# Kernel optimization log

Measured on AMD Instinct MI355X. Metric: run time of the kernel, lower is better.

The kernel has to match this reference:

```python
import jax, jax.numpy as jnp
import numpy as np

F_FRAMES = 128   # number of frames (seq_start_end rows)
P_PEDS = 32      # pedestrians per frame (uniform)
B = F_FRAMES * P_PEDS
E, H, BN, PM, M = 64, 128, 1024, 512, 1024
PRED_LEN = 12


def setup_inputs() -> dict:
    key = jax.random.key(0)
    ks = jax.random.split(key, 20)
    n = lambda k, s, sc=0.05: (jax.random.normal(k, s) * sc).astype(jnp.float32)
    starts = jnp.arange(F_FRAMES, dtype=jnp.int32) * P_PEDS
    seq_start_end = jnp.stack([starts, starts + P_PEDS], axis=1)
    return {
        "h0": n(ks[0], (1, B, H), 1.0),
        "c0": n(ks[1], (1, B, H), 1.0),
        "obs_final_pos": n(ks[2], (B, 2), 1.0),
        "obs_final_pos_rel": n(ks[3], (B, 2), 1.0),
        "W_emb": n(ks[4], (2, E)), "b_emb": jnp.zeros((E,), jnp.float32),
        "W_ih": n(ks[5], (4 * H, E)), "W_hh": n(ks[6], (4 * H, H)),
        "b_ih": jnp.zeros((4 * H,), jnp.float32), "b_hh": jnp.zeros((4 * H,), jnp.float32),
        "W_pos": n(ks[7], (H, 2)), "b_pos": jnp.zeros((2,), jnp.float32),
        "W_pe": n(ks[8], (2, E)), "b_pe": jnp.zeros((E,), jnp.float32),
        "W_p1": n(ks[9], (E + H, PM)), "b_p1": jnp.zeros((PM,), jnp.float32),
        "W_p2": n(ks[10], (PM, BN)), "b_p2": jnp.zeros((BN,), jnp.float32),
        "W_m1": n(ks[11], (H + BN, M)), "b_m1": jnp.zeros((M,), jnp.float32),
        "W_m2": n(ks[12], (M, H)), "b_m2": jnp.zeros((H,), jnp.float32),
        "seq_start_end": seq_start_end,
    }


def reference(h0, c0, obs_final_pos, obs_final_pos_rel,
              W_emb, b_emb, W_ih, W_hh, b_ih, b_hh, W_pos, b_pos,
              W_pe, b_pe, W_p1, b_p1, W_p2, b_p2, W_m1, b_m1, W_m2, b_m2,
              seq_start_end):
    Bn = h0.shape[1]
    F = seq_start_end.shape[0]
    P = Bn // F  # uniform frame size
    h, c = h0[0], c0[0]
    x0 = obs_final_pos_rel @ W_emb + b_emb  # decoder input embedding

    def step(carry, _):
        x, h, c, last_pos = carry
        # LSTM cell (PyTorch gate order i,f,g,o)
        gates = x @ W_ih.T + h @ W_hh.T + b_ih + b_hh  # (B, 4H)
        i, f, g, o = jnp.split(gates, 4, axis=-1)
        i, f, o = jax.nn.sigmoid(i), jax.nn.sigmoid(f), jax.nn.sigmoid(o)
        c_new = f * c + i * jnp.tanh(g)
        h_new = o * jnp.tanh(c_new)
        rel_pos = h_new @ W_pos + b_pos
        curr_pos = rel_pos + last_pos
        # PoolNet: per-frame pairwise rel-pos embed + MLP + max over neighbours j
        pos = curr_pos.reshape(F, P, 2)
        hf = h_new.reshape(F, P, H)
        rel = pos[:, None, :, :] - pos[:, :, None, :]  # rel[f,i,j] = pos_j - pos_i
        e = rel @ W_pe + b_pe  # (F,P,P,E)
        feat = jnp.concatenate(
            [e, jnp.broadcast_to(hf[:, None], (F, P, P, H))], axis=-1)  # h of j
        z = jax.nn.relu(feat @ W_p1 + b_p1)
        z = jax.nn.relu(z @ W_p2 + b_p2)  # (F,P,P,BN)
        pool_h = z.max(axis=2).reshape(Bn, BN)
        # hidden refresh MLP
        mi = jnp.concatenate([h_new, pool_h], axis=-1)
        nh = jax.nn.relu(mi @ W_m1 + b_m1)
        nh = jax.nn.relu(nh @ W_m2 + b_m2)
        x_new = rel_pos @ W_emb + b_emb
        return (x_new, nh, c_new, curr_pos), (curr_pos, rel_pos)

    _, (pred_seq, pred_seq_rel) = jax.lax.scan(
        jax.checkpoint(step), (x0, h, c, obs_final_pos), None, length=PRED_LEN)
    return pred_seq, pred_seq_rel
```

## Files before the change

kernel.cpp:

```cpp
#include <hip/hip_runtime.h>

#define NB 4096
#define HD 128
#define ED 64
#define NF 128
#define NP 32
#define TSTEPS 12

typedef __attribute__((ext_vector_type(8))) short short8;
typedef __attribute__((ext_vector_type(8))) __bf16 bf16x8;
typedef __attribute__((ext_vector_type(8))) _Float16 f16x8;
typedef __attribute__((ext_vector_type(4))) float f32x4;

#define MFMA16(a, b, c) __builtin_amdgcn_mfma_f32_16x16x32_bf16((a), (b), (c), 0, 0, 0)
#define MFMAH(a, b, c)  __builtin_amdgcn_mfma_f32_16x16x32_f16((a), (b), (c), 0, 0, 0)

__device__ __forceinline__ unsigned short f2bf(float f) {
  unsigned int x = __float_as_uint(f);
  x += 0x7fffu + ((x >> 16) & 1u);
  return (unsigned short)(x >> 16);
}

__device__ __forceinline__ float sigm(float x) { return 1.0f / (1.0f + expf(-x)); }


__global__ __launch_bounds__(256) void k_transpose_bf(const float* __restrict__ W,
                                                      unsigned short* __restrict__ Wt,
                                                      int K, int N) {
  __shared__ float t[32][33];
  int nb = blockIdx.x * 32, kb = blockIdx.y * 32;
  int tx = threadIdx.x & 31, ty = threadIdx.x >> 5;
  #pragma unroll
  for (int r = 0; r < 32; r += 8)
    t[ty + r][tx] = W[(size_t)(kb + ty + r) * N + nb + tx];
  __syncthreads();
  #pragma unroll
  for (int r = 0; r < 32; r += 8)
    Wt[(size_t)(nb + ty + r) * K + kb + tx] = f2bf(t[tx][ty + r]);
}

__global__ __launch_bounds__(256) void k_transpose_f16(const float* __restrict__ W,
                                                       _Float16* __restrict__ Wt,
                                                       int K, int N) {
  __shared__ float t[32][33];
  int nb = blockIdx.x * 32, kb = blockIdx.y * 32;
  int tx = threadIdx.x & 31, ty = threadIdx.x >> 5;
  #pragma unroll
  for (int r = 0; r < 32; r += 8)
    t[ty + r][tx] = W[(size_t)(kb + ty + r) * N + nb + tx];
  __syncthreads();
  #pragma unroll
  for (int r = 0; r < 32; r += 8)
    Wt[(size_t)(nb + ty + r) * K + kb + tx] = (_Float16)t[tx][ty + r];
}

__global__ __launch_bounds__(256) void k_pack_lstm_w(const float* __restrict__ Wih,
                                                     const float* __restrict__ Whh,
                                                     float* __restrict__ WihT,
                                                     float* __restrict__ WhhT) {
  int idx = blockIdx.x * 256 + threadIdx.x;
  if (idx < 64 * 512) { int k = idx >> 9, n = idx & 511; WihT[idx] = Wih[n * 64 + k]; }
  if (idx < 128 * 512) { int k = idx >> 9, n = idx & 511; WhhT[idx] = Whh[n * 128 + k]; }
}

__global__ __launch_bounds__(256) void k_pack_wpp(const float* __restrict__ Wpe,
                                                  const float* __restrict__ bpe,
                                                  const float* __restrict__ Wp1,
                                                  const float* __restrict__ bp1,
                                                  float* __restrict__ Wpp,
                                                  float* __restrict__ cvec) {
  int n = blockIdx.x * 256 + threadIdx.x;
  if (n >= 512) return;
  float s0 = 0.f, s1 = 0.f, sc = 0.f;
  for (int k = 0; k < 64; ++k) {
    float w = Wp1[k * 512 + n];
    s0 += Wpe[k] * w;
    s1 += Wpe[64 + k] * w;
    sc += bpe[k] * w;
  }
  Wpp[n * 2] = s0; Wpp[n * 2 + 1] = s1; cvec[n] = sc + bp1[n];
}

__global__ __launch_bounds__(256) void k_x0(const float* __restrict__ ofr,
                                            const float* __restrict__ Wemb,
                                            const float* __restrict__ bemb,
                                            float* __restrict__ x) {
  int idx = blockIdx.x * 256 + threadIdx.x;
  if (idx >= NB * ED) return;
  int row = idx >> 6, e = idx & 63;
  x[idx] = bemb[e] + ofr[row * 2] * Wemb[e] + ofr[row * 2 + 1] * Wemb[64 + e];
}


__global__ __launch_bounds__(256) void k1_lstm(
    const float* __restrict__ x, const float* __restrict__ hin, const float* __restrict__ cin,
    const float* __restrict__ WihT, const float* __restrict__ WhhT,
    const float* __restrict__ bih, const float* __restrict__ bhh,
    const float* __restrict__ Wpos, const float* __restrict__ bpos,
    const float* __restrict__ Wemb, const float* __restrict__ bemb,
    const float* __restrict__ lastpos,
    float* __restrict__ cout, float* __restrict__ hnew, unsigned short* __restrict__ mi,
    float* __restrict__ posout, float* __restrict__ xout,
    float* __restrict__ outc, float* __restrict__ outr) {
  __shared__ float xh[8][192];
  __shared__ float hnl[8][128];
  __shared__ float rp[8][2];
  int tid = threadIdx.x;
  int r0 = blockIdx.x * 8;
  for (int idx = tid; idx < 8 * 192; idx += 256) {
    int r = idx / 192, k = idx % 192;
    xh[r][k] = (k < 64) ? x[(r0 + r) * 64 + k] : hin[(r0 + r) * 128 + (k - 64)];
  }
  __syncthreads();
  int j = tid & 127, rg = tid >> 7;
  float acc0[4], acc1[4], acc2[4], acc3[4];
  {
    float b0 = bih[j] + bhh[j];
    float b1 = bih[128 + j] + bhh[128 + j];
    float b2 = bih[256 + j] + bhh[256 + j];
    float b3 = bih[384 + j] + bhh[384 + j];
    #pragma unroll
    for (int r = 0; r < 4; ++r) { acc0[r] = b0; acc1[r] = b1; acc2[r] = b2; acc3[r] = b3; }
  }
  for (int k = 0; k < 64; ++k) {
    float w0 = WihT[k * 512 + j], w1 = WihT[k * 512 + 128 + j],
          w2 = WihT[k * 512 + 256 + j], w3 = WihT[k * 512 + 384 + j];
    #pragma unroll
    for (int r = 0; r < 4; ++r) {
      float xv = xh[rg * 4 + r][k];
      acc0[r] += w0 * xv; acc1[r] += w1 * xv; acc2[r] += w2 * xv; acc3[r] += w3 * xv;
    }
  }
  for (int k = 0; k < 128; ++k) {
    float w0 = WhhT[k * 512 + j], w1 = WhhT[k * 512 + 128 + j],
          w2 = WhhT[k * 512 + 256 + j], w3 = WhhT[k * 512 + 384 + j];
    #pragma unroll
    for (int r = 0; r < 4; ++r) {
      float hv = xh[rg * 4 + r][64 + k];
      acc0[r] += w0 * hv; acc1[r] += w1 * hv; acc2[r] += w2 * hv; acc3[r] += w3 * hv;
    }
  }
  #pragma unroll
  for (int r = 0; r < 4; ++r) {
    int row = r0 + rg * 4 + r;
    float ig = sigm(acc0[r]), fg = sigm(acc1[r]), gg = tanhf(acc2[r]), og = sigm(acc3[r]);
    float cn = fg * cin[row * 128 + j] + ig * gg;
    float hv = og * tanhf(cn);
    cout[row * 128 + j] = cn;
    hnew[row * 128 + j] = hv;
    mi[(size_t)row * 1152 + j] = f2bf(hv);
    hnl[rg * 4 + r][j] = hv;
  }
  __syncthreads();
  if (tid < 16) {
    int r = tid >> 1, d = tid & 1, row = r0 + r;
    float s = bpos[d];
    for (int k = 0; k < 128; ++k) s += hnl[r][k] * Wpos[k * 2 + d];
    float cur = s + lastpos[row * 2 + d];
    rp[r][d] = s;
    posout[row * 2 + d] = cur;
    outc[row * 2 + d] = cur;
    outr[row * 2 + d] = s;
  }
  __syncthreads();
  for (int idx = tid; idx < 8 * 64; idx += 256) {
    int r = idx >> 6, e = idx & 63;
    xout[(r0 + r) * 64 + e] = bemb[e] + rp[r][0] * Wemb[e] + rp[r][1] * Wemb[64 + e];
  }
}

__global__ __launch_bounds__(256) void k2_uv(
    const float* __restrict__ hnew, const float* __restrict__ pos,
    const float* __restrict__ Wp1, const float* __restrict__ Wpp,
    const float* __restrict__ cvec, _Float16* __restrict__ u16, _Float16* __restrict__ v16) {
  __shared__ float h8[8][128];
  __shared__ float p8[8][2];
  int tid = threadIdx.x, r0 = blockIdx.x * 8;
  for (int idx = tid; idx < 1024; idx += 256) {
    int r = idx >> 7, k = idx & 127;
    h8[r][k] = hnew[(r0 + r) * 128 + k];
  }
  if (tid < 16) p8[tid >> 1][tid & 1] = pos[r0 * 2 + tid];
  __syncthreads();
  int n = tid, n2 = tid + 256;
  float aA[8], aB[8];
  #pragma unroll
  for (int r = 0; r < 8; ++r) { aA[r] = 0.f; aB[r] = 0.f; }
  for (int k = 0; k < 128; ++k) {
    float wA = Wp1[(64 + k) * 512 + n], wB = Wp1[(64 + k) * 512 + n2];
    #pragma unroll
    for (int r = 0; r < 8; ++r) { aA[r] += wA * h8[r][k]; aB[r] += wB * h8[r][k]; }
  }
  float wp0A = Wpp[n * 2], wp1A = Wpp[n * 2 + 1], cA = cvec[n];
  float wp0B = Wpp[n2 * 2], wp1B = Wpp[n2 * 2 + 1], cB = cvec[n2];
  #pragma unroll
  for (int r = 0; r < 8; ++r) {
    int row = r0 + r;
    float t0 = p8[r][0] * wp0A + p8[r][1] * wp1A;
    v16[(size_t)row * 512 + n] = (_Float16)t0;
    u16[(size_t)row * 512 + n] = (_Float16)(t0 + aA[r] + cA);
    float t1 = p8[r][0] * wp0B + p8[r][1] * wp1B;
    v16[(size_t)row * 512 + n2] = (_Float16)t1;
    u16[(size_t)row * 512 + n2] = (_Float16)(t1 + aB[r] + cB);
  }
}

#define ULD 520
#define BLD 40
__global__ __launch_bounds__(512, 4) void k3_pool(
    const _Float16* __restrict__ u16, const _Float16* __restrict__ v16,
    const _Float16* __restrict__ Bt, const float* __restrict__ bp2,
    unsigned short* __restrict__ mi) {
  __shared__ _Float16 u_lds[32 * ULD];
  __shared__ _Float16 v_lds[4 * ULD];
  __shared__ _Float16 b_lds[2][256 * BLD];
  int bid = blockIdx.x;
  int f = bid & 127, iblk = (bid >> 7) & 7, nblk = bid >> 10;
  int tid = threadIdx.x, wid = tid >> 6, lane = tid & 63;
  int c = lane & 15, q = lane >> 4;
  int i_loc = wid >> 1;
  int nh = wid & 1;

  #pragma unroll
  for (int t = 0; t < 4; ++t) {
    int unit = tid + t * 512;
    int row = unit >> 6, colu = unit & 63;
    f16x8 val = *(const f16x8*)(u16 + (size_t)(f * 32 + row) * 512 + colu * 8);
    *(f16x8*)(u_lds + row * ULD + colu * 8) = val;
  }
  if (tid < 256) {
    int row = tid >> 6, colu = tid & 63;
    f16x8 val = *(const f16x8*)(v16 + (size_t)(f * 32 + iblk * 4 + row) * 512 + colu * 8);
    *(f16x8*)(v_lds + row * ULD + colu * 8) = val;
  }
  int br = tid >> 1, bh = tid & 1;
  const _Float16* gbase = Bt + (size_t)(nblk * 256 + br) * 512 + bh * 16;
  {
    f16x8 b0 = *(const f16x8*)(gbase);
    f16x8 b1 = *(const f16x8*)(gbase + 8);
    _Float16* d = b_lds[0] + br * BLD + bh * 16;
    *(f16x8*)(d) = b0;
    *(f16x8*)(d + 8) = b1;
  }
  __syncthreads();

  f32x4 acc[2][8];
  #pragma unroll
  for (int a = 0; a < 2; ++a)
    #pragma unroll
    for (int b = 0; b < 8; ++b) acc[a][b] = (f32x4){0.f, 0.f, 0.f, 0.f};

  const _Float16* up0 = u_lds + c * ULD;
  const _Float16* up1 = u_lds + (c + 16) * ULD;
  const _Float16* vp  = v_lds + i_loc * ULD;
  const _Float16* blb = b_lds[0] + (nh * 128 + c) * BLD + q * 8;
  int bufstride = 256 * BLD;

  #pragma unroll
  for (int ks = 0; ks < 16; ++ks) {
    f16x8 s0, s1;
    if (ks < 15) {
      const _Float16* gb = gbase + (ks + 1) * 32;
      s0 = *(const f16x8*)(gb);
      s1 = *(const f16x8*)(gb + 8);
    }
    int k0 = ks * 32 + q * 8;
    f16x8 uv0 = *(const f16x8*)(up0 + k0);
    f16x8 uv1 = *(const f16x8*)(up1 + k0);
    f16x8 vv  = *(const f16x8*)(vp + k0);
    f16x8 a0 = uv0 - vv;
    f16x8 a1 = uv1 - vv;
    a0 = __builtin_elementwise_max(a0, (f16x8)(_Float16)0);
    a1 = __builtin_elementwise_max(a1, (f16x8)(_Float16)0);
    const _Float16* bl = blb + (ks & 1) * bufstride;
    #pragma unroll
    for (int nt = 0; nt < 8; ++nt) {
      f16x8 bf = *(const f16x8*)(bl + nt * 16 * BLD);
      acc[0][nt] = MFMAH(a0, bf, acc[0][nt]);
      acc[1][nt] = MFMAH(a1, bf, acc[1][nt]);
    }
    __syncthreads();
    if (ks < 15) {
      _Float16* d = b_lds[(ks + 1) & 1] + br * BLD + bh * 16;
      *(f16x8*)(d) = s0;
      *(f16x8*)(d + 8) = s1;
    }
    __syncthreads();
  }

  int i = iblk * 4 + i_loc;
  #pragma unroll
  for (int nt = 0; nt < 8; ++nt) {
    float m = acc[0][nt][0];
    #pragma unroll
    for (int r = 0; r < 4; ++r) { m = fmaxf(m, acc[0][nt][r]); m = fmaxf(m, acc[1][nt][r]); }
    m = fmaxf(m, __shfl_xor(m, 16));
    m = fmaxf(m, __shfl_xor(m, 32));
    int n = nblk * 256 + nh * 128 + nt * 16 + c;
    m = fmaxf(m + bp2[n], 0.0f);
    if (q == 0) mi[(size_t)(f * 32 + i) * 1152 + 128 + n] = f2bf(m);
  }
}

__global__ __launch_bounds__(512) void k4_mlp1(
    const unsigned short* __restrict__ mi, const unsigned short* __restrict__ Wt,
    const float* __restrict__ bm1, unsigned short* __restrict__ nh1) {
  int bid = blockIdx.x;
  int mb = bid & 63, nb = bid >> 6;
  int tid = threadIdx.x, wid = tid >> 6, lane = tid & 63;
  int row0 = mb * 64 + (wid >> 2) * 32;
  int nc0 = nb * 256 + (wid & 3) * 64;
  int c = lane & 15, q = lane >> 4;
  const unsigned short* a0p = mi + (size_t)(row0 + c) * 1152;
  const unsigned short* a1p = a0p + 16 * 1152;
  const unsigned short* bb = Wt + (size_t)(nc0 + c) * 1152;
  f32x4 acc[2][4];
  #pragma unroll
  for (int a = 0; a < 2; ++a)
    #pragma unroll
    for (int b = 0; b < 4; ++b) acc[a][b] = (f32x4){0.f, 0.f, 0.f, 0.f};
  for (int ks = 0; ks < 36; ++ks) {
    int k0 = ks * 32 + q * 8;
    bf16x8 a0 = *(const bf16x8*)(a0p + k0);
    bf16x8 a1 = *(const bf16x8*)(a1p + k0);
    #pragma unroll
    for (int nt = 0; nt < 4; ++nt) {
      bf16x8 bf = *(const bf16x8*)(bb + (size_t)nt * 16 * 1152 + k0);
      acc[0][nt] = MFMA16(a0, bf, acc[0][nt]);
      acc[1][nt] = MFMA16(a1, bf, acc[1][nt]);
    }
  }
  #pragma unroll
  for (int mt = 0; mt < 2; ++mt)
    #pragma unroll
    for (int nt = 0; nt < 4; ++nt)
      #pragma unroll
      for (int r = 0; r < 4; ++r) {
        int row = row0 + mt * 16 + q * 4 + r;
        int col = nc0 + nt * 16 + c;
        float val = fmaxf(acc[mt][nt][r] + bm1[col], 0.f);
        nh1[(size_t)row * 1024 + col] = f2bf(val);
      }
}

__global__ __launch_bounds__(512) void k5_mlp2(
    const unsigned short* __restrict__ nh1, const unsigned short* __restrict__ Wt,
    const float* __restrict__ bm2, float* __restrict__ hout) {
  int bid = blockIdx.x;
  int tid = threadIdx.x, wid = tid >> 6, lane = tid & 63;
  int row0 = bid * 64 + (wid >> 1) * 16;
  int nc0 = (wid & 1) * 64;
  int c = lane & 15, q = lane >> 4;
  const unsigned short* ap = nh1 + (size_t)(row0 + c) * 1024;
  const unsigned short* bb = Wt + (size_t)(nc0 + c) * 1024;
  f32x4 acc[4];
  #pragma unroll
  for (int b = 0; b < 4; ++b) acc[b] = (f32x4){0.f, 0.f, 0.f, 0.f};
  for (int ks = 0; ks < 32; ++ks) {
    int k0 = ks * 32 + q * 8;
    bf16x8 a = *(const bf16x8*)(ap + k0);
    #pragma unroll
    for (int nt = 0; nt < 4; ++nt) {
      bf16x8 bf = *(const bf16x8*)(bb + (size_t)nt * 16 * 1024 + k0);
      acc[nt] = MFMA16(a, bf, acc[nt]);
    }
  }
  #pragma unroll
  for (int nt = 0; nt < 4; ++nt)
    #pragma unroll
    for (int r = 0; r < 4; ++r) {
      int row = row0 + q * 4 + r;
      int col = nc0 + nt * 16 + c;
      hout[(size_t)row * 128 + col] = fmaxf(acc[nt][r] + bm2[col], 0.f);
    }
}


extern "C" void kernel_launch(void* const* d_in, const int* in_sizes, int n_in,
                              void* d_out, int out_size, void* d_ws, size_t ws_size,
                              hipStream_t stream) {
  const float* h0   = (const float*)d_in[0];
  const float* c0   = (const float*)d_in[1];
  const float* ofp  = (const float*)d_in[2];
  const float* ofr  = (const float*)d_in[3];
  const float* Wemb = (const float*)d_in[4];
  const float* bemb = (const float*)d_in[5];
  const float* Wih  = (const float*)d_in[6];
  const float* Whh  = (const float*)d_in[7];
  const float* bih  = (const float*)d_in[8];
  const float* bhh  = (const float*)d_in[9];
  const float* Wpos = (const float*)d_in[10];
  const float* bpos = (const float*)d_in[11];
  const float* Wpe  = (const float*)d_in[12];
  const float* bpe  = (const float*)d_in[13];
  const float* Wp1  = (const float*)d_in[14];
  const float* bp1  = (const float*)d_in[15];
  const float* Wp2  = (const float*)d_in[16];
  const float* bp2  = (const float*)d_in[17];
  const float* Wm1  = (const float*)d_in[18];
  const float* bm1  = (const float*)d_in[19];
  const float* Wm2  = (const float*)d_in[20];
  const float* bm2  = (const float*)d_in[21];

  char* ws = (char*)d_ws;
  size_t off = 0;
  auto alloc = [&](size_t bytes) {
    char* p = ws + off;
    off += (bytes + 255) & ~(size_t)255;
    return p;
  };
  float* h    = (float*)alloc((size_t)NB * HD * 4);
  float* cst  = (float*)alloc((size_t)NB * HD * 4);
  float* hnew = (float*)alloc((size_t)NB * HD * 4);
  float* xbuf = (float*)alloc((size_t)NB * ED * 4);
  float* pos  = (float*)alloc((size_t)NB * 2 * 4);
  _Float16* u16 = (_Float16*)alloc((size_t)NB * 512 * 2);
  _Float16* v16 = (_Float16*)alloc((size_t)NB * 512 * 2);
  unsigned short* mi   = (unsigned short*)alloc((size_t)NB * 1152 * 2);
  unsigned short* nh1  = (unsigned short*)alloc((size_t)NB * 1024 * 2);
  float* WihT = (float*)alloc(64 * 512 * 4);
  float* WhhT = (float*)alloc(128 * 512 * 4);
  float* Wpp  = (float*)alloc(512 * 2 * 4);
  float* cvec = (float*)alloc(512 * 4);
  _Float16* Bt2 = (_Float16*)alloc((size_t)1024 * 512 * 2);
  unsigned short* Wm1t = (unsigned short*)alloc((size_t)1024 * 1152 * 2);
  unsigned short* Wm2t = (unsigned short*)alloc((size_t)128 * 1024 * 2);

  float* outc = (float*)d_out;
  float* outr = outc + (size_t)TSTEPS * NB * 2;

  k_pack_lstm_w<<<256, 256, 0, stream>>>(Wih, Whh, WihT, WhhT);
  k_pack_wpp<<<2, 256, 0, stream>>>(Wpe, bpe, Wp1, bp1, Wpp, cvec);
  k_transpose_f16<<<dim3(1024 / 32, 512 / 32), 256, 0, stream>>>(Wp2, Bt2, 512, 1024);
  k_transpose_bf<<<dim3(1024 / 32, 1152 / 32), 256, 0, stream>>>(Wm1, Wm1t, 1152, 1024);
  k_transpose_bf<<<dim3(128 / 32, 1024 / 32), 256, 0, stream>>>(Wm2, Wm2t, 1024, 128);
  k_x0<<<NB * ED / 256, 256, 0, stream>>>(ofr, Wemb, bemb, xbuf);

  for (int t = 0; t < TSTEPS; ++t) {
    const float* hin = (t == 0) ? h0 : h;
    const float* cin = (t == 0) ? c0 : cst;
    const float* lp  = (t == 0) ? ofp : pos;
    k1_lstm<<<NB / 8, 256, 0, stream>>>(xbuf, hin, cin, WihT, WhhT, bih, bhh, Wpos, bpos,
                                        Wemb, bemb, lp, cst, hnew, mi, pos, xbuf,
                                        outc + (size_t)t * NB * 2, outr + (size_t)t * NB * 2);
    k2_uv<<<NB / 8, 256, 0, stream>>>(hnew, pos, Wp1, Wpp, cvec, u16, v16);
    k3_pool<<<4096, 512, 0, stream>>>(u16, v16, Bt2, bp2, mi);
    k4_mlp1<<<256, 512, 0, stream>>>(mi, Wm1t, bm1, nh1);
    k5_mlp2<<<64, 512, 0, stream>>>(nh1, Wm2t, bm2, h);
  }
}
```

Before: 3.366 ms.

## Retile pooling GEMM onto 32x32x16 MFMA and parallelize Wpos projection

The pooling kernel now uses 32x32x16 f16 MFMA. Each block handles 8 query pedestrians by 128 output columns over a 3D grid, reusing each B fragment across 4 accumulators. It drops one of the two barriers per k-step and raises wave priority around the MFMA section. The LSTM kernel's rel-pos projection now uses 256 threads with shuffle reductions instead of 16 serial threads. The pooling kernel's accumulator footprint and register pressure grow, and the new per-block tile shape changes how much u/v data is reloaded.

Result: slower. 3.688 ms (+9.5%).

```diff
diff --git a/kernel.cpp b/kernel.cpp
--- a/kernel.cpp
+++ b/kernel.cpp
@@ -11,9 +11,10 @@
 typedef __attribute__((ext_vector_type(8))) __bf16 bf16x8;
 typedef __attribute__((ext_vector_type(8))) _Float16 f16x8;
 typedef __attribute__((ext_vector_type(4))) float f32x4;
+typedef __attribute__((ext_vector_type(16))) float f32x16;
 
 #define MFMA16(a, b, c) __builtin_amdgcn_mfma_f32_16x16x32_bf16((a), (b), (c), 0, 0, 0)
-#define MFMAH(a, b, c)  __builtin_amdgcn_mfma_f32_16x16x32_f16((a), (b), (c), 0, 0, 0)
+#define MFMA32H(a, b, c) __builtin_amdgcn_mfma_f32_32x32x16_f16((a), (b), (c), 0, 0, 0)
 
 __device__ __forceinline__ unsigned short f2bf(float f) {
   unsigned int x = __float_as_uint(f);
@@ -22,6 +23,10 @@
 }
 
 __device__ __forceinline__ float sigm(float x) { return 1.0f / (1.0f + expf(-x)); }
+
+__device__ __forceinline__ f16x8 relu8(f16x8 x) {
+  return __builtin_elementwise_max(x, (f16x8)(_Float16)0);
+}
 
 
 __global__ __launch_bounds__(256) void k_transpose_bf(const float* __restrict__ W,
@@ -152,15 +157,26 @@
     hnl[rg * 4 + r][j] = hv;
   }
   __syncthreads();
-  if (tid < 16) {
-    int r = tid >> 1, d = tid & 1, row = r0 + r;
-    float s = bpos[d];
-    for (int k = 0; k < 128; ++k) s += hnl[r][k] * Wpos[k * 2 + d];
-    float cur = s + lastpos[row * 2 + d];
-    rp[r][d] = s;
-    posout[row * 2 + d] = cur;
-    outc[row * 2 + d] = cur;
-    outr[row * 2 + d] = s;
+  if (tid < 256) {
+    int r = tid >> 5;
+    int d = (tid >> 4) & 1;
+    int l = tid & 15;
+    float s = 0.f;
+    #pragma unroll
+    for (int k = l; k < 128; k += 16) s += hnl[r][k] * Wpos[k * 2 + d];
+    s += __shfl_xor(s, 1);
+    s += __shfl_xor(s, 2);
+    s += __shfl_xor(s, 4);
+    s += __shfl_xor(s, 8);
+    if (l == 0) {
+      int row = r0 + r;
+      float rel = s + bpos[d];
+      float cur = rel + lastpos[row * 2 + d];
+      rp[r][d] = rel;
+      posout[row * 2 + d] = cur;
+      outc[row * 2 + d] = cur;
+      outr[row * 2 + d] = rel;
+    }
   }
   __syncthreads();
   for (int idx = tid; idx < 8 * 64; idx += 256) {
@@ -212,93 +228,81 @@
     const _Float16* __restrict__ Bt, const float* __restrict__ bp2,
     unsigned short* __restrict__ mi) {
   __shared__ _Float16 u_lds[32 * ULD];
-  __shared__ _Float16 v_lds[4 * ULD];
-  __shared__ _Float16 b_lds[2][256 * BLD];
-  int bid = blockIdx.x;
-  int f = bid & 127, iblk = (bid >> 7) & 7, nblk = bid >> 10;
+  __shared__ _Float16 v_lds[8 * ULD];
+  __shared__ _Float16 b_lds[2][128 * BLD];
+  int f = blockIdx.x, ig = blockIdx.y, ng = blockIdx.z;
   int tid = threadIdx.x, wid = tid >> 6, lane = tid & 63;
-  int c = lane & 15, q = lane >> 4;
-  int i_loc = wid >> 1;
-  int nh = wid & 1;
-
-  #pragma unroll
-  for (int t = 0; t < 4; ++t) {
-    int unit = tid + t * 512;
-    int row = unit >> 6, colu = unit & 63;
-    f16x8 val = *(const f16x8*)(u16 + (size_t)(f * 32 + row) * 512 + colu * 8);
-    *(f16x8*)(u_lds + row * ULD + colu * 8) = val;
-  }
-  if (tid < 256) {
-    int row = tid >> 6, colu = tid & 63;
-    f16x8 val = *(const f16x8*)(v16 + (size_t)(f * 32 + iblk * 4 + row) * 512 + colu * 8);
-    *(f16x8*)(v_lds + row * ULD + colu * 8) = val;
-  }
-  int br = tid >> 1, bh = tid & 1;
-  const _Float16* gbase = Bt + (size_t)(nblk * 256 + br) * 512 + bh * 16;
+  int ip = wid >> 2;
+  int nh = wid & 3;
+  int r32 = lane & 31, hi = lane >> 5;
+
+  #pragma unroll
+  for (int it = 0; it < 4; ++it) {
+    int unit = tid + it * 512;
+    int row = unit >> 6, seg = unit & 63;
+    *(f16x8*)(u_lds + row * ULD + seg * 8) =
+        *(const f16x8*)(u16 + (size_t)(f * 32 + row) * 512 + seg * 8);
+  }
   {
-    f16x8 b0 = *(const f16x8*)(gbase);
-    f16x8 b1 = *(const f16x8*)(gbase + 8);
-    _Float16* d = b_lds[0] + br * BLD + bh * 16;
-    *(f16x8*)(d) = b0;
-    *(f16x8*)(d + 8) = b1;
-  }
-  __syncthreads();
-
-  f32x4 acc[2][8];
-  #pragma unroll
-  for (int a = 0; a < 2; ++a)
-    #pragma unroll
-    for (int b = 0; b < 8; ++b) acc[a][b] = (f32x4){0.f, 0.f, 0.f, 0.f};
-
-  const _Float16* up0 = u_lds + c * ULD;
-  const _Float16* up1 = u_lds + (c + 16) * ULD;
-  const _Float16* vp  = v_lds + i_loc * ULD;
-  const _Float16* blb = b_lds[0] + (nh * 128 + c) * BLD + q * 8;
-  int bufstride = 256 * BLD;
-
-  #pragma unroll
+    int row = tid >> 6, seg = tid & 63;
+    *(f16x8*)(v_lds + row * ULD + seg * 8) =
+        *(const f16x8*)(v16 + (size_t)(f * 32 + ig * 8 + row) * 512 + seg * 8);
+  }
+  int brow = tid >> 2, bseg = tid & 3;
+  const _Float16* gb = Bt + (size_t)(ng * 128 + brow) * 512 + bseg * 8;
+  *(f16x8*)(b_lds[0] + brow * BLD + bseg * 8) = *(const f16x8*)(gb);
+  __syncthreads();
+
+  f32x16 acc[4];
+  #pragma unroll
+  for (int ii = 0; ii < 4; ++ii)
+    #pragma unroll
+    for (int r = 0; r < 16; ++r) acc[ii][r] = 0.f;
+
+  const _Float16* up = u_lds + r32 * ULD + hi * 8;
+  const _Float16* vp = v_lds + (size_t)ip * 4 * ULD + hi * 8;
+  const _Float16* bp = b_lds[0] + (nh * 32 + r32) * BLD + hi * 8;
+
+  #pragma unroll 2
   for (int ks = 0; ks < 16; ++ks) {
-    f16x8 s0, s1;
-    if (ks < 15) {
-      const _Float16* gb = gbase + (ks + 1) * 32;
-      s0 = *(const f16x8*)(gb);
-      s1 = *(const f16x8*)(gb + 8);
-    }
-    int k0 = ks * 32 + q * 8;
-    f16x8 uv0 = *(const f16x8*)(up0 + k0);
-    f16x8 uv1 = *(const f16x8*)(up1 + k0);
-    f16x8 vv  = *(const f16x8*)(vp + k0);
-    f16x8 a0 = uv0 - vv;
-    f16x8 a1 = uv1 - vv;
-    a0 = __builtin_elementwise_max(a0, (f16x8)(_Float16)0);
-    a1 = __builtin_elementwise_max(a1, (f16x8)(_Float16)0);
-    const _Float16* bl = blb + (ks & 1) * bufstride;
-    #pragma unroll
-    for (int nt = 0; nt < 8; ++nt) {
-      f16x8 bf = *(const f16x8*)(bl + nt * 16 * BLD);
-      acc[0][nt] = MFMAH(a0, bf, acc[0][nt]);
-      acc[1][nt] = MFMAH(a1, bf, acc[1][nt]);
-    }
+    f16x8 s0;
+    if (ks < 15) s0 = *(const f16x8*)(gb + (ks + 1) * 32);
+    const _Float16* bcur = bp + (ks & 1) * (128 * BLD);
+    int kb = ks * 32;
+    __builtin_amdgcn_s_setprio(1);
+    #pragma unroll
+    for (int kf = 0; kf < 2; ++kf) {
+      int ko = kb + kf * 16;
+      f16x8 uf = *(const f16x8*)(up + ko);
+      f16x8 bf = *(const f16x8*)(bcur + kf * 16);
+      f16x8 a0 = relu8(uf - *(const f16x8*)(vp + ko));
+      f16x8 a1 = relu8(uf - *(const f16x8*)(vp + ULD + ko));
+      f16x8 a2 = relu8(uf - *(const f16x8*)(vp + 2 * ULD + ko));
+      f16x8 a3 = relu8(uf - *(const f16x8*)(vp + 3 * ULD + ko));
+      acc[0] = MFMA32H(a0, bf, acc[0]);
+      acc[1] = MFMA32H(a1, bf, acc[1]);
+      acc[2] = MFMA32H(a2, bf, acc[2]);
+      acc[3] = MFMA32H(a3, bf, acc[3]);
+    }
+    __builtin_amdgcn_s_setprio(0);
+    if (ks < 15)
+      *(f16x8*)(b_lds[(ks + 1) & 1] + brow * BLD + bseg * 8) = s0;
     __syncthreads();
-    if (ks < 15) {
-      _Float16* d = b_lds[(ks + 1) & 1] + br * BLD + bh * 16;
-      *(f16x8*)(d) = s0;
-      *(f16x8*)(d + 8) = s1;
-    }
-    __syncthreads();
-  }
-
-  int i = iblk * 4 + i_loc;
-  #pragma unroll
-  for (int nt = 0; nt < 8; ++nt) {
-    float m = acc[0][nt][0];
-    #pragma unroll
-    for (int r = 0; r < 4; ++r) { m = fmaxf(m, acc[0][nt][r]); m = fmaxf(m, acc[1][nt][r]); }
-    m = fmaxf(m, __shfl_xor(m, 16));
+  }
+
+  int col = ng * 128 + nh * 32 + r32;
+  float bias = bp2[col];
+  #pragma unroll
+  for (int ii = 0; ii < 4; ++ii) {
+    float m = acc[ii][0];
+    #pragma unroll
+    for (int r = 1; r < 16; ++r) m = fmaxf(m, acc[ii][r]);
     m = fmaxf(m, __shfl_xor(m, 32));
-    int n = nblk * 256 + nh * 128 + nt * 16 + c;
-    m = fmaxf(m + bp2[n], 0.0f);
-    if (q == 0) mi[(size_t)(f * 32 + i) * 1152 + 128 + n] = f2bf(m);
+    if (hi == 0) {
+      int rowg = f * 32 + ig * 8 + ip * 4 + ii;
+      float val = fmaxf(m + bias, 0.f);
+      mi[(size_t)rowg * 1152 + 128 + col] = f2bf(val);
+    }
   }
 }
 
@@ -444,7 +448,7 @@
                                         Wemb, bemb, lp, cst, hnew, mi, pos, xbuf,
                                         outc + (size_t)t * NB * 2, outr + (size_t)t * NB * 2);
     k2_uv<<<NB / 8, 256, 0, stream>>>(hnew, pos, Wp1, Wpp, cvec, u16, v16);
-    k3_pool<<<4096, 512, 0, stream>>>(u16, v16, Bt2, bp2, mi);
+    k3_pool<<<dim3(128, 4, 8), 512, 0, stream>>>(u16, v16, Bt2, bp2, mi);
     k4_mlp1<<<256, 512, 0, stream>>>(mi, Wm1t, bm1, nh1);
     k5_mlp2<<<64, 512, 0, stream>>>(nh1, Wm2t, bm2, h);
   }
```
